# Optimization experiments

Hardware: AMD Instinct MI355X
Metric: run time of the kernel (lower is better)

Reference implementation:

```python
import jax, jax.numpy as jnp
import numpy as np

B, S, D, H = 2, 4096, 512, 8
HD = D // H


def setup_inputs() -> dict:
    key = jax.random.key(0)
    ks = jax.random.split(key, 11)
    s = 1.0 / np.sqrt(D)
    return {
        "queries": jax.random.normal(ks[0], (B, S, D), jnp.float32),
        "keys": jax.random.normal(ks[1], (B, S, D), jnp.float32),
        "values": jax.random.normal(ks[2], (B, S, D), jnp.float32),
        "Wq": jax.random.normal(ks[3], (D, D), jnp.float32) * s,
        "bq": jnp.zeros((D,), jnp.float32),
        "Wk": jax.random.normal(ks[4], (D, D), jnp.float32) * s,
        "bk": jnp.zeros((D,), jnp.float32),
        "Wv": jax.random.normal(ks[5], (D, D), jnp.float32) * s,
        "bv": jnp.zeros((D,), jnp.float32),
        "Wo": jax.random.normal(ks[6], (D, D), jnp.float32) * s,
        "bo": jnp.zeros((D,), jnp.float32),
    }


def reference(queries, keys, values, Wq, bq, Wk, bk, Wv, bv, Wo, bo):
    b = queries.shape[0]
    # Linear projections (torch Linear: x @ W.T + b; here W stored as [in, out])
    q = (queries @ Wq + bq).reshape(b, -1, H, HD)   # [B, Sq, H, HD]
    k = (keys @ Wk + bk).reshape(b, -1, H, HD)       # [B, Sk, H, HD]
    v = (values @ Wv + bv).reshape(b, -1, H, HD)     # [B, Sk, H, HD]
    logits = jnp.einsum('bqhd,bkhd->bhqk', q, k) / jnp.sqrt(jnp.float32(HD))
    attn = jax.nn.softmax(logits, axis=-1)           # [B, H, Sq, Sk]  (dropout_rate=0 -> identity)
    ctx = jnp.einsum('bhqk,bkhd->bqhd', attn, v).reshape(b, -1, H * HD)
    return ctx @ Wo + bo
```

## Files before the change

### kernel.cpp

```cpp
#include <hip/hip_runtime.h>
#include <hip/hip_bf16.h>

constexpr int B_  = 2;
constexpr int S_  = 4096;
constexpr int D_  = 512;
constexpr int H_  = 8;
constexpr int HD_ = 64;
constexpr int M_  = B_ * S_;

typedef __attribute__((ext_vector_type(8))) short short8;
typedef __attribute__((ext_vector_type(4))) short short4v;
typedef __attribute__((ext_vector_type(4))) float floatx4;

static __device__ __forceinline__ unsigned short f2bf(float f) {
    union { float f; unsigned u; } v; v.f = f;
    unsigned r = v.u + 0x7fffu + ((v.u >> 16) & 1u);
    return (unsigned short)(r >> 16);
}

static __device__ __forceinline__ unsigned pk2bf(float a, float b) {
#if __has_builtin(__builtin_amdgcn_cvt_pk_bf16_f32)
    typedef __attribute__((ext_vector_type(2))) __bf16 bf16x2_t;
    union { bf16x2_t v; unsigned u; } u;
    u.v = __builtin_amdgcn_cvt_pk_bf16_f32(a, b);
    return u.u;
#else
    return (unsigned)f2bf(a) | ((unsigned)f2bf(b) << 16);
#endif
}

#if __has_builtin(__builtin_amdgcn_exp2f)
#define EXP2(x) __builtin_amdgcn_exp2f(x)
#else
#define EXP2(x) exp2f(x)
#endif

#if __has_builtin(__builtin_amdgcn_mfma_f32_16x16x16bf16_1k)
static __device__ __forceinline__ floatx4 mfma16k(short4v a, short4v b, floatx4 c) {
    return __builtin_amdgcn_mfma_f32_16x16x16bf16_1k(a, b, c, 0, 0, 0);
}
#else
static __device__ __forceinline__ floatx4 mfma16k(short4v a, short4v b, floatx4 c) {
    short8 a8 = {a[0], a[1], a[2], a[3], 0, 0, 0, 0};
    short8 b8 = {b[0], b[1], b[2], b[3], 0, 0, 0, 0};
    return __builtin_amdgcn_mfma_f32_16x16x32_bf16(a8, b8, c, 0, 0, 0);
}
#endif

#define QSCALE 0.18033688011110204f

static __device__ __forceinline__ void gl_lds16(const void* g, void* l) {
    typedef __attribute__((address_space(1))) const unsigned GU;
    typedef __attribute__((address_space(3))) unsigned LU;
    __builtin_amdgcn_global_load_lds((GU*)g, (LU*)l, 16, 0, 0);
}

__global__ __launch_bounds__(256) void xcast_kernel(
    const float* __restrict__ Xq, const float* __restrict__ Xk, const float* __restrict__ Xv,
    unsigned short* __restrict__ Y) {
    const int z = blockIdx.z;
    const float* X = z == 0 ? Xq : (z == 1 ? Xk : Xv);
    unsigned short* Yz = Y + (size_t)z * M_ * D_;
    const int n8 = M_ * D_ / 8;
    int i = blockIdx.x * 256 + threadIdx.x;
    const int stride = gridDim.x * 256;
    for (; i < n8; i += stride) {
        float4 a = *(const float4*)&X[(size_t)i * 8];
        float4 b = *(const float4*)&X[(size_t)i * 8 + 4];
        union { short8 s; unsigned u[4]; } p;
        p.u[0] = pk2bf(a.x, a.y); p.u[1] = pk2bf(a.z, a.w);
        p.u[2] = pk2bf(b.x, b.y); p.u[3] = pk2bf(b.z, b.w);
        *(short8*)&Yz[(size_t)i * 8] = p.s;
    }
}

__global__ __launch_bounds__(256) void wtrans_kernel(
    const float* __restrict__ Wq, const float* __restrict__ Wk,
    const float* __restrict__ Wv, const float* __restrict__ Wo,
    unsigned short* __restrict__ Tq, unsigned short* __restrict__ Tk,
    unsigned short* __restrict__ Tv, unsigned short* __restrict__ To) {
    const int z = blockIdx.z;
    const float* W = z == 0 ? Wq : (z == 1 ? Wk : (z == 2 ? Wv : Wo));
    unsigned short* Wt = z == 0 ? Tq : (z == 1 ? Tk : (z == 2 ? Tv : To));
    __shared__ float T[64][65];
    const int t = threadIdx.x;
    const int k0 = blockIdx.x * 64, n0 = blockIdx.y * 64;
#pragma unroll
    for (int i = 0; i < 4; ++i) {
        const int flat = t + 256 * i;
        const int kr = flat >> 4, nc = (flat & 15) * 4;
        float4 v = *(const float4*)&W[(size_t)(k0 + kr) * 512 + n0 + nc];
        T[kr][nc] = v.x; T[kr][nc + 1] = v.y; T[kr][nc + 2] = v.z; T[kr][nc + 3] = v.w;
    }
    __syncthreads();
#pragma unroll
    for (int i = 0; i < 4; ++i) {
        const int flat = t + 256 * i;
        const int nr = flat >> 4, kc = (flat & 15) * 4;
        ushort4 o4;
        o4.x = f2bf(T[kc][nr]);     o4.y = f2bf(T[kc + 1][nr]);
        o4.z = f2bf(T[kc + 2][nr]); o4.w = f2bf(T[kc + 3][nr]);
        *(ushort4*)&Wt[(size_t)(n0 + nr) * 512 + k0 + kc] = o4;
    }
}

template <int MODE>
__global__ __launch_bounds__(256, 3) void gemm_kernel(
    const unsigned short* __restrict__ Ab,
    const unsigned short* __restrict__ Wt,
    const float* __restrict__ b0, const float* __restrict__ b1, const float* __restrict__ b2,
    unsigned short* __restrict__ o0, unsigned short* __restrict__ o1,
    unsigned short* __restrict__ o2, float* __restrict__ of) {
    __shared__ unsigned short As[128 * 64];
    __shared__ unsigned short Bs[128 * 64];

    const int tid  = threadIdx.x;
    const int w    = tid >> 6;
    const int lane = tid & 63;
    const int n0   = blockIdx.x * 128;
    const int m0   = blockIdx.y * 128;
    const int lm   = lane & 15;
    const int lq   = lane >> 4;
    const int lm7  = lm & 7;
    const int wm   = (w >> 1) * 64;
    const int wn   = (w & 1) * 64;

    const int z = MODE == 0 ? (n0 >> 9) : 0;
    const unsigned short* A = MODE == 0 ? Ab + (size_t)z * M_ * D_ : Ab;

    const int srow = lane >> 3;
    const int slc  = ((lane & 7) ^ (srow & 7)) * 8;

    floatx4 acc[4][4];
#pragma unroll
    for (int i = 0; i < 4; ++i)
#pragma unroll
        for (int j = 0; j < 4; ++j) acc[i][j] = (floatx4)0.0f;

    for (int kb = 0; kb < 8; ++kb) {
        const int k0 = kb * 64;
        __syncthreads();
#pragma unroll
        for (int it = 0; it < 4; ++it) {
            const int r8 = w * 32 + it * 8;
            gl_lds16(&A [(size_t)(m0 + r8 + srow) * 512 + k0 + slc], &As[r8 * 64]);
            gl_lds16(&Wt[(size_t)(n0 + r8 + srow) * 512 + k0 + slc], &Bs[r8 * 64]);
        }
        __syncthreads();

        short8 af[2][4], bf[2][4];
#pragma unroll
        for (int ks = 0; ks < 2; ++ks)
#pragma unroll
            for (int i = 0; i < 4; ++i) {
                const int cc = ((ks * 4 + lq) ^ lm7) * 8;
                af[ks][i] = *(const short8*)&As[(wm + i * 16 + lm) * 64 + cc];
                bf[ks][i] = *(const short8*)&Bs[(wn + i * 16 + lm) * 64 + cc];
            }
#pragma unroll
        for (int ks = 0; ks < 2; ++ks)
#pragma unroll
            for (int mi = 0; mi < 4; ++mi)
#pragma unroll
                for (int ni = 0; ni < 4; ++ni)
                    acc[mi][ni] = __builtin_amdgcn_mfma_f32_16x16x32_bf16(
                        af[ks][mi], bf[ks][ni], acc[mi][ni], 0, 0, 0);
    }

    const float* bias = MODE == 0 ? (z == 0 ? b0 : (z == 1 ? b1 : b2)) : b0;
    const float scale = (MODE == 0 && z == 0) ? QSCALE : 1.0f;
    const int nl0 = n0 & 511;

    float bias_n[4];
#pragma unroll
    for (int ni = 0; ni < 4; ++ni) bias_n[ni] = bias[nl0 + wn + ni * 16 + lm];

#pragma unroll
    for (int mi = 0; mi < 4; ++mi) {
#pragma unroll
        for (int ni = 0; ni < 4; ++ni) {
            if (MODE == 1) {
                const int gn = n0 + wn + ni * 16 + lm;
#pragma unroll
                for (int r = 0; r < 4; ++r) {
                    const int gm = m0 + wm + mi * 16 + lq * 4 + r;
                    of[(size_t)gm * 512 + gn] = acc[mi][ni][r] + bias_n[ni];
                }
            } else {
                const int gnl = nl0 + wn + ni * 16 + lm;
                if (z == 2) {
                    const int h = gnl >> 6, hd = gnl & 63;
                    const int gm = m0 + wm + mi * 16 + lq * 4;
                    const int b = gm >> 12, s = gm & 4095;
                    union { ushort4 s4; uint2 u; } o4;
                    o4.u.x = pk2bf(acc[mi][ni][0] + bias_n[ni], acc[mi][ni][1] + bias_n[ni]);
                    o4.u.y = pk2bf(acc[mi][ni][2] + bias_n[ni], acc[mi][ni][3] + bias_n[ni]);
                    *(ushort4*)&o2[(((size_t)(b * 8 + h)) * 64 + hd) * 4096 + s] = o4.s4;
                } else {
                    unsigned short* out = z == 0 ? o0 : o1;
#pragma unroll
                    for (int r = 0; r < 4; ++r) {
                        const int gm = m0 + wm + mi * 16 + lq * 4 + r;
                        out[(size_t)gm * 512 + gnl] =
                            f2bf((acc[mi][ni][r] + bias_n[ni]) * scale);
                    }
                }
            }
        }
    }
}

__global__ __launch_bounds__(256) void flash_kernel(
    const unsigned short* __restrict__ Q, const unsigned short* __restrict__ K,
    const unsigned short* __restrict__ Vt, unsigned short* __restrict__ ctx) {
    __shared__ unsigned short Ks[2][64 * 64];
    __shared__ unsigned short Vs[2][64 * 64];

    const int tid = threadIdx.x;
    const int w   = tid >> 6;
    const int l   = tid & 63;
    const int lm  = l & 15;
    const int lq  = l >> 4;
    const int lm7 = lm & 7;
    const int q0  = blockIdx.x * 128;
    const int bh  = blockIdx.y;
    const int b   = bh >> 3, h = bh & 7;

    const unsigned short* Vg = Vt + (size_t)bh * HD_ * S_;
    const size_t rowbase = (size_t)b * 4096;

    short8 qf[2][2];
#pragma unroll
    for (int qn = 0; qn < 2; ++qn) {
        const unsigned short* qp =
            &Q[(rowbase + q0 + w * 32 + qn * 16 + lm) * 512 + h * 64];
        qf[qn][0] = *(const short8*)(qp + lq * 8);
        qf[qn][1] = *(const short8*)(qp + 32 + lq * 8);
    }

    short4v ones4;
#pragma unroll
    for (int j = 0; j < 4; ++j) ones4[j] = (short)0x3F80;

    floatx4 o[2][4];
#pragma unroll
    for (int qn = 0; qn < 2; ++qn)
#pragma unroll
        for (int i = 0; i < 4; ++i) o[qn][i] = (floatx4)0.0f;
    floatx4 ls[2];
    ls[0] = (floatx4)0.0f; ls[1] = (floatx4)0.0f;

    const int srow = l >> 3;
    const int slc  = ((l & 7) ^ (srow & 7)) * 8;

#define STAGE(T0, BUF)                                                         \
    {                                                                          \
        _Pragma("unroll") for (int it = 0; it < 2; ++it) {                     \
            const int r8 = w * 16 + it * 8;                                    \
            gl_lds16(&K[(rowbase + (T0) + r8 + srow) * 512 + h * 64 + slc],    \
                     &Ks[BUF][r8 * 64]);                                       \
            gl_lds16(&Vg[(size_t)(r8 + srow) * 4096 + (T0) + slc],            \
                     &Vs[BUF][r8 * 64]);                                       \
        }                                                                      \
    }

    STAGE(0, 0);
    __syncthreads();

    for (int kt = 0; kt < 64; ++kt) {
        const int cur = kt & 1;
        if (kt < 63) STAGE((kt + 1) * 64, cur ^ 1);

        short8 kf[2][4];
#pragma unroll
        for (int ks = 0; ks < 2; ++ks)
#pragma unroll
            for (int ni = 0; ni < 4; ++ni)
                kf[ks][ni] = *(const short8*)&Ks[cur][(ni * 16 + lm) * 64 +
                                                      (((ks * 4 + lq) ^ lm7) * 8)];
        short4v vfr[4][4];
#pragma unroll
        for (int mt = 0; mt < 4; ++mt)
#pragma unroll
            for (int ni = 0; ni < 4; ++ni)
                vfr[mt][ni] = *(const short4v*)&Vs[cur][(mt * 16 + lm) * 64 +
                                                        (((ni * 2 + (lq >> 1)) ^ lm7) * 8) +
                                                        (lq & 1) * 4];

#pragma unroll
        for (int qn = 0; qn < 2; ++qn) {
            floatx4 sf[4];
#pragma unroll
            for (int ni = 0; ni < 4; ++ni) sf[ni] = (floatx4)0.0f;
#pragma unroll
            for (int ks = 0; ks < 2; ++ks)
#pragma unroll
                for (int ni = 0; ni < 4; ++ni)
                    sf[ni] = __builtin_amdgcn_mfma_f32_16x16x32_bf16(
                        kf[ks][ni], qf[qn][ks], sf[ni], 0, 0, 0);

            short4v pp[4];
#pragma unroll
            for (int ni = 0; ni < 4; ++ni) {
                union { short4v s; unsigned u[2]; } t;
                t.u[0] = pk2bf(EXP2(sf[ni][0]), EXP2(sf[ni][1]));
                t.u[1] = pk2bf(EXP2(sf[ni][2]), EXP2(sf[ni][3]));
                pp[ni] = t.s;
            }
#pragma unroll
            for (int ni = 0; ni < 4; ++ni) {
                ls[qn] = mfma16k(ones4, pp[ni], ls[qn]);
#pragma unroll
                for (int mt = 0; mt < 4; ++mt)
                    o[qn][mt] = mfma16k(vfr[mt][ni], pp[ni], o[qn][mt]);
            }
        }
        __syncthreads();
    }

#pragma unroll
    for (int qn = 0; qn < 2; ++qn) {
        const float inv = 1.0f / ls[qn][0];
        const int q = q0 + w * 32 + qn * 16 + lm;
        const size_t rb = (rowbase + q) * 512 + h * 64;
#pragma unroll
        for (int mt = 0; mt < 4; ++mt) {
            union { ushort4 s; uint2 u; } o4;
            o4.u.x = pk2bf(o[qn][mt][0] * inv, o[qn][mt][1] * inv);
            o4.u.y = pk2bf(o[qn][mt][2] * inv, o[qn][mt][3] * inv);
            *(ushort4*)&ctx[rb + mt * 16 + lq * 4] = o4.s;
        }
    }
}

extern "C" void kernel_launch(void* const* d_in, const int* in_sizes, int n_in,
                              void* d_out, int out_size, void* d_ws, size_t ws_size,
                              hipStream_t stream) {
    const float* queries = (const float*)d_in[0];
    const float* keys    = (const float*)d_in[1];
    const float* values  = (const float*)d_in[2];
    const float* Wq = (const float*)d_in[3];
    const float* bq = (const float*)d_in[4];
    const float* Wk = (const float*)d_in[5];
    const float* bk = (const float*)d_in[6];
    const float* Wv = (const float*)d_in[7];
    const float* bv = (const float*)d_in[8];
    const float* Wo = (const float*)d_in[9];
    const float* bo = (const float*)d_in[10];

    unsigned short* xb    = (unsigned short*)d_ws;
    unsigned short* wsctx = xb;
    unsigned short* wsq   = xb   + (size_t)3 * M_ * D_;
    unsigned short* wsk   = wsq  + (size_t)M_ * D_;
    unsigned short* wsvt  = wsk  + (size_t)M_ * D_;
    unsigned short* wtq   = wsvt + (size_t)M_ * D_;
    unsigned short* wtk   = wtq  + (size_t)D_ * D_;
    unsigned short* wtv   = wtk  + (size_t)D_ * D_;
    unsigned short* wto   = wtv  + (size_t)D_ * D_;

    xcast_kernel<<<dim3(1024, 1, 3), dim3(256), 0, stream>>>(queries, keys, values, xb);
    wtrans_kernel<<<dim3(8, 8, 4), dim3(256), 0, stream>>>(
        Wq, Wk, Wv, Wo, wtq, wtk, wtv, wto);

    gemm_kernel<0><<<dim3(12, 64), dim3(256), 0, stream>>>(
        xb, wtq, bq, bk, bv, wsq, wsk, wsvt, nullptr);

    flash_kernel<<<dim3(S_ / 128, B_ * H_), dim3(256), 0, stream>>>(
        wsq, wsk, wsvt, wsctx);

    gemm_kernel<1><<<dim3(4, 64), dim3(256), 0, stream>>>(
        wsctx, wto, bo, nullptr, nullptr, nullptr, nullptr, nullptr, (float*)d_out);
}
```

Baseline: 265.2 us.

## Merge prep kernels and use K=32 MFMA for PV via LDS-staged P

```diff
diff --git a/kernel.cpp b/kernel.cpp
--- a/kernel.cpp
+++ b/kernel.cpp
@@ -9,7 +9,6 @@
 constexpr int M_  = B_ * S_;
 
 typedef __attribute__((ext_vector_type(8))) short short8;
-typedef __attribute__((ext_vector_type(4))) short short4v;
 typedef __attribute__((ext_vector_type(4))) float floatx4;
 
 static __device__ __forceinline__ unsigned short f2bf(float f) {
@@ -35,18 +34,6 @@
 #define EXP2(x) exp2f(x)
 #endif
 
-#if __has_builtin(__builtin_amdgcn_mfma_f32_16x16x16bf16_1k)
-static __device__ __forceinline__ floatx4 mfma16k(short4v a, short4v b, floatx4 c) {
-    return __builtin_amdgcn_mfma_f32_16x16x16bf16_1k(a, b, c, 0, 0, 0);
-}
-#else
-static __device__ __forceinline__ floatx4 mfma16k(short4v a, short4v b, floatx4 c) {
-    short8 a8 = {a[0], a[1], a[2], a[3], 0, 0, 0, 0};
-    short8 b8 = {b[0], b[1], b[2], b[3], 0, 0, 0, 0};
-    return __builtin_amdgcn_mfma_f32_16x16x32_bf16(a8, b8, c, 0, 0, 0);
-}
-#endif
-
 #define QSCALE 0.18033688011110204f
 
 static __device__ __forceinline__ void gl_lds16(const void* g, void* l) {
@@ -55,52 +42,55 @@
     __builtin_amdgcn_global_load_lds((GU*)g, (LU*)l, 16, 0, 0);
 }
 
-__global__ __launch_bounds__(256) void xcast_kernel(
+__global__ __launch_bounds__(256) void prep_kernel(
     const float* __restrict__ Xq, const float* __restrict__ Xk, const float* __restrict__ Xv,
-    unsigned short* __restrict__ Y) {
-    const int z = blockIdx.z;
-    const float* X = z == 0 ? Xq : (z == 1 ? Xk : Xv);
-    unsigned short* Yz = Y + (size_t)z * M_ * D_;
-    const int n8 = M_ * D_ / 8;
-    int i = blockIdx.x * 256 + threadIdx.x;
-    const int stride = gridDim.x * 256;
-    for (; i < n8; i += stride) {
-        float4 a = *(const float4*)&X[(size_t)i * 8];
-        float4 b = *(const float4*)&X[(size_t)i * 8 + 4];
-        union { short8 s; unsigned u[4]; } p;
-        p.u[0] = pk2bf(a.x, a.y); p.u[1] = pk2bf(a.z, a.w);
-        p.u[2] = pk2bf(b.x, b.y); p.u[3] = pk2bf(b.z, b.w);
-        *(short8*)&Yz[(size_t)i * 8] = p.s;
-    }
-}
-
-__global__ __launch_bounds__(256) void wtrans_kernel(
     const float* __restrict__ Wq, const float* __restrict__ Wk,
     const float* __restrict__ Wv, const float* __restrict__ Wo,
-    unsigned short* __restrict__ Tq, unsigned short* __restrict__ Tk,
-    unsigned short* __restrict__ Tv, unsigned short* __restrict__ To) {
-    const int z = blockIdx.z;
-    const float* W = z == 0 ? Wq : (z == 1 ? Wk : (z == 2 ? Wv : Wo));
-    unsigned short* Wt = z == 0 ? Tq : (z == 1 ? Tk : (z == 2 ? Tv : To));
-    __shared__ float T[64][65];
-    const int t = threadIdx.x;
-    const int k0 = blockIdx.x * 64, n0 = blockIdx.y * 64;
-#pragma unroll
-    for (int i = 0; i < 4; ++i) {
-        const int flat = t + 256 * i;
-        const int kr = flat >> 4, nc = (flat & 15) * 4;
-        float4 v = *(const float4*)&W[(size_t)(k0 + kr) * 512 + n0 + nc];
-        T[kr][nc] = v.x; T[kr][nc + 1] = v.y; T[kr][nc + 2] = v.z; T[kr][nc + 3] = v.w;
-    }
-    __syncthreads();
-#pragma unroll
-    for (int i = 0; i < 4; ++i) {
-        const int flat = t + 256 * i;
-        const int nr = flat >> 4, kc = (flat & 15) * 4;
-        ushort4 o4;
-        o4.x = f2bf(T[kc][nr]);     o4.y = f2bf(T[kc + 1][nr]);
-        o4.z = f2bf(T[kc + 2][nr]); o4.w = f2bf(T[kc + 3][nr]);
-        *(ushort4*)&Wt[(size_t)(n0 + nr) * 512 + k0 + kc] = o4;
+    unsigned short* __restrict__ Y,
+    unsigned short* __restrict__ T) {
+    const int bid = blockIdx.x;
+    const int t   = threadIdx.x;
+    __shared__ float Tt[64][65];
+
+    if (bid < 1536) {
+        const int z   = bid / 512;
+        const int blk = bid - z * 512;
+        const float* X = z == 0 ? Xq : (z == 1 ? Xk : Xv);
+        unsigned short* Yz = Y + (size_t)z * M_ * D_;
+        const int n8 = M_ * D_ / 8;
+        for (int i = blk * 256 + t; i < n8; i += 512 * 256) {
+            float4 a = *(const float4*)&X[(size_t)i * 8];
+            float4 b = *(const float4*)&X[(size_t)i * 8 + 4];
+            union { short8 s; unsigned u[4]; } p;
+            p.u[0] = pk2bf(a.x, a.y); p.u[1] = pk2bf(a.z, a.w);
+            p.u[2] = pk2bf(b.x, b.y); p.u[3] = pk2bf(b.z, b.w);
+            *(short8*)&Yz[(size_t)i * 8] = p.s;
+        }
+    } else {
+        const int b2 = bid - 1536;
+        const int z  = b2 >> 6;
+        const int rm = b2 & 63;
+        const int k0 = (rm >> 3) * 64, n0 = (rm & 7) * 64;
+        const float* W = z == 0 ? Wq : (z == 1 ? Wk : (z == 2 ? Wv : Wo));
+        unsigned short* Wt = T + (size_t)z * D_ * D_;
+#pragma unroll
+        for (int i = 0; i < 4; ++i) {
+            const int flat = t + 256 * i;
+            const int kr = flat >> 4, nc = (flat & 15) * 4;
+            float4 v = *(const float4*)&W[(size_t)(k0 + kr) * 512 + n0 + nc];
+            Tt[kr][nc] = v.x; Tt[kr][nc + 1] = v.y;
+            Tt[kr][nc + 2] = v.z; Tt[kr][nc + 3] = v.w;
+        }
+        __syncthreads();
+#pragma unroll
+        for (int i = 0; i < 4; ++i) {
+            const int flat = t + 256 * i;
+            const int nr = flat >> 4, kc = (flat & 15) * 4;
+            ushort4 o4;
+            o4.x = f2bf(Tt[kc][nr]);     o4.y = f2bf(Tt[kc + 1][nr]);
+            o4.z = f2bf(Tt[kc + 2][nr]); o4.w = f2bf(Tt[kc + 3][nr]);
+            *(ushort4*)&Wt[(size_t)(n0 + nr) * 512 + k0 + kc] = o4;
+        }
     }
 }
 
@@ -215,6 +205,7 @@
     const unsigned short* __restrict__ Vt, unsigned short* __restrict__ ctx) {
     __shared__ unsigned short Ks[2][64 * 64];
     __shared__ unsigned short Vs[2][64 * 64];
+    __shared__ unsigned short Ps[4][16 * 64];
 
     const int tid = threadIdx.x;
     const int w   = tid >> 6;
@@ -238,9 +229,9 @@
         qf[qn][1] = *(const short8*)(qp + 32 + lq * 8);
     }
 
-    short4v ones4;
-#pragma unroll
-    for (int j = 0; j < 4; ++j) ones4[j] = (short)0x3F80;
+    short8 ones8;
+#pragma unroll
+    for (int j = 0; j < 8; ++j) ones8[j] = (short)0x3F80;
 
     floatx4 o[2][4];
 #pragma unroll
@@ -267,6 +258,8 @@
     STAGE(0, 0);
     __syncthreads();
 
+    unsigned short* Pw = &Ps[w][0];
+
     for (int kt = 0; kt < 64; ++kt) {
         const int cur = kt & 1;
         if (kt < 63) STAGE((kt + 1) * 64, cur ^ 1);
@@ -278,14 +271,13 @@
             for (int ni = 0; ni < 4; ++ni)
                 kf[ks][ni] = *(const short8*)&Ks[cur][(ni * 16 + lm) * 64 +
                                                       (((ks * 4 + lq) ^ lm7) * 8)];
-        short4v vfr[4][4];
-#pragma unroll
-        for (int mt = 0; mt < 4; ++mt)
-#pragma unroll
-            for (int ni = 0; ni < 4; ++ni)
-                vfr[mt][ni] = *(const short4v*)&Vs[cur][(mt * 16 + lm) * 64 +
-                                                        (((ni * 2 + (lq >> 1)) ^ lm7) * 8) +
-                                                        (lq & 1) * 4];
+        short8 vf[2][4];
+#pragma unroll
+        for (int c = 0; c < 2; ++c)
+#pragma unroll
+            for (int mt = 0; mt < 4; ++mt)
+                vf[c][mt] = *(const short8*)&Vs[cur][(mt * 16 + lm) * 64 +
+                                                     (((c * 4 + lq) ^ lm7) * 8)];
 
 #pragma unroll
         for (int qn = 0; qn < 2; ++qn) {
@@ -299,20 +291,21 @@
                     sf[ni] = __builtin_amdgcn_mfma_f32_16x16x32_bf16(
                         kf[ks][ni], qf[qn][ks], sf[ni], 0, 0, 0);
 
-            short4v pp[4];
 #pragma unroll
             for (int ni = 0; ni < 4; ++ni) {
-                union { short4v s; unsigned u[2]; } t;
-                t.u[0] = pk2bf(EXP2(sf[ni][0]), EXP2(sf[ni][1]));
-                t.u[1] = pk2bf(EXP2(sf[ni][2]), EXP2(sf[ni][3]));
-                pp[ni] = t.s;
+                uint2 pv;
+                pv.x = pk2bf(EXP2(sf[ni][0]), EXP2(sf[ni][1]));
+                pv.y = pk2bf(EXP2(sf[ni][2]), EXP2(sf[ni][3]));
+                *(uint2*)&Pw[lm * 64 + (((ni * 2 + (lq >> 1)) ^ lm7) * 8) + (lq & 1) * 4] = pv;
             }
 #pragma unroll
-            for (int ni = 0; ni < 4; ++ni) {
-                ls[qn] = mfma16k(ones4, pp[ni], ls[qn]);
+            for (int c = 0; c < 2; ++c) {
+                short8 pf = *(const short8*)&Pw[lm * 64 + (((c * 4 + lq) ^ lm7) * 8)];
+                ls[qn] = __builtin_amdgcn_mfma_f32_16x16x32_bf16(ones8, pf, ls[qn], 0, 0, 0);
 #pragma unroll
                 for (int mt = 0; mt < 4; ++mt)
-                    o[qn][mt] = mfma16k(vfr[mt][ni], pp[ni], o[qn][mt]);
+                    o[qn][mt] = __builtin_amdgcn_mfma_f32_16x16x32_bf16(
+                        vf[c][mt], pf, o[qn][mt], 0, 0, 0);
             }
         }
         __syncthreads();
@@ -353,17 +346,14 @@
     unsigned short* wsq   = xb   + (size_t)3 * M_ * D_;
     unsigned short* wsk   = wsq  + (size_t)M_ * D_;
     unsigned short* wsvt  = wsk  + (size_t)M_ * D_;
-    unsigned short* wtq   = wsvt + (size_t)M_ * D_;
-    unsigned short* wtk   = wtq  + (size_t)D_ * D_;
-    unsigned short* wtv   = wtk  + (size_t)D_ * D_;
-    unsigned short* wto   = wtv  + (size_t)D_ * D_;
-
-    xcast_kernel<<<dim3(1024, 1, 3), dim3(256), 0, stream>>>(queries, keys, values, xb);
-    wtrans_kernel<<<dim3(8, 8, 4), dim3(256), 0, stream>>>(
-        Wq, Wk, Wv, Wo, wtq, wtk, wtv, wto);
+    unsigned short* wt    = wsvt + (size_t)M_ * D_;
+    unsigned short* wto   = wt   + (size_t)3 * D_ * D_;
+
+    prep_kernel<<<dim3(1792), dim3(256), 0, stream>>>(
+        queries, keys, values, Wq, Wk, Wv, Wo, xb, wt);
 
     gemm_kernel<0><<<dim3(12, 64), dim3(256), 0, stream>>>(
-        xb, wtq, bq, bk, bv, wsq, wsk, wsvt, nullptr);
+        xb, wt, bq, bk, bv, wsq, wsk, wsvt, nullptr);
 
     flash_kernel<<<dim3(S_ / 128, B_ * H_), dim3(256), 0, stream>>>(
         wsq, wsk, wsvt, wsctx);
```

Measured after the change: 268.3 us. Within noise of the previous version (+1.2%).
